# Optimization experiments

Measured on AMD Instinct MI355X. Metric: run time of the kernel, lower is better.

The kernel has to match this reference:

```python
import jax, jax.numpy as jnp
import numpy as np

B, N, D = 256, 256, 256
DELTA_BEARING = 5.0
DELTA_HEADING = 5.0
N_HEAD = int(360 / DELTA_HEADING)   # 72
N_BEAR = int(360 / DELTA_BEARING)   # 72
DOMAIN_PARAM = 2.0
EPS = 1e-14


def setup_inputs() -> dict:
    key = jax.random.key(0)
    ks = jax.random.split(key, 8)
    hidden_state = jax.random.normal(ks[0], (B, N, D), dtype=jnp.float32)
    distance_matrix = jax.random.uniform(ks[1], (B, N, N), dtype=jnp.float32) * 10.0
    bearing_matrix = jax.random.uniform(ks[2], (B, N, N), dtype=jnp.float32) * 360.0
    heading_matrix = jax.random.uniform(ks[3], (B, N, N), dtype=jnp.float32) * 360.0
    sequence_mask = (jax.random.uniform(ks[4], (B, N)) > 0.1).astype(jnp.float32)
    domain = jnp.full((N_HEAD, N_BEAR), DOMAIN_PARAM, dtype=jnp.float32)
    lim = 1.0 / np.sqrt(2 * D)
    W = jax.random.uniform(ks[5], (D, 2 * D), minval=-lim, maxval=lim, dtype=jnp.float32)
    b = jax.random.uniform(ks[6], (D,), minval=-lim, maxval=lim, dtype=jnp.float32)
    return {"hidden_state": hidden_state, "distance_matrix": distance_matrix,
            "bearing_matrix": bearing_matrix, "heading_matrix": heading_matrix,
            "sequence_mask": sequence_mask, "domain": domain, "W": W, "b": b}


def _compute_weights(domain, distance_matrix, bearing_matrix, heading_matrix, sequence_mask):
    # domain lookup indices from heading/bearing bins
    idx1 = jnp.clip(jnp.floor((heading_matrix + DELTA_HEADING / 2) / DELTA_HEADING), 0, N_HEAD - 1).astype(jnp.int32)
    idx2 = jnp.clip(jnp.floor((bearing_matrix + DELTA_BEARING / 2) / DELTA_BEARING), 0, N_BEAR - 1).astype(jnp.int32)
    w = jax.nn.relu(domain[idx1, idx2] - distance_matrix)  # (B,N,N)
    # pairwise sequence mask and no-self-attention mask
    wm = sequence_mask[:, :, None] * sequence_mask[:, None, :]  # (B,N,N)
    ped = 1.0 - jnp.eye(w.shape[1], dtype=w.dtype)               # (N,N)
    valid = (ped[None, :, :] * wm) > 0
    w = jnp.where(valid, w, 0.0)
    # masked softmax over dim=2: zeros are treated as masked, epsilon-stabilized
    mask = (w != 0).astype(w.dtype)
    masked_exps = jnp.exp(w) * mask + EPS
    w = masked_exps / (masked_exps.sum(axis=2, keepdims=True) + EPS)
    return jnp.where(valid, w, 0.0)


def reference(hidden_state, distance_matrix, bearing_matrix, heading_matrix, sequence_mask, domain, W, b):
    weights = _compute_weights(domain, distance_matrix, bearing_matrix, heading_matrix, sequence_mask)
    weighted_hidden = jnp.einsum('bij,bjd->bid', weights, hidden_state)  # (B,N,D)
    cat = jnp.concatenate([weighted_hidden, hidden_state], axis=-1)       # (B,N,2D)
    return jnp.einsum('bnk,dk->bnd', cat, W) + b
```

## Files before the change

### kernel.cpp

```cpp
#include <hip/hip_runtime.h>
#include <hip/hip_bf16.h>


typedef __attribute__((ext_vector_type(4))) float  f32x4;
typedef __attribute__((ext_vector_type(8))) short  bf16x8;
typedef __attribute__((ext_vector_type(4))) short  bf16x4;

#define EPSC 1e-14f

__device__ __forceinline__ short f2bf(float v) {
  __hip_bfloat16 h = __float2bfloat16(v);
  return *reinterpret_cast<short*>(&h);
}

__global__ void k0_pack(const float* __restrict__ W, short* __restrict__ Wbf) {
  int idx = blockIdx.x * 256 + threadIdx.x;
  f32x4 v = *(const f32x4*)(W + (size_t)idx * 4);
  bf16x4 pk;
  pk[0] = f2bf(v[0]); pk[1] = f2bf(v[1]); pk[2] = f2bf(v[2]); pk[3] = f2bf(v[3]);
  *(bf16x4*)(Wbf + (size_t)idx * 4) = pk;
}

__global__ __launch_bounds__(512) void k1_proj(
    const float* __restrict__ H, const short* __restrict__ Wbf,
    short* __restrict__ P1T) {
  extern __shared__ char sm[];
  char* sA = sm;
  char* sB = sm + 9216;
  const int t  = threadIdx.x;
  const int n0 = blockIdx.x * 64;
  const int b  = n0 >> 8;
  const int jb = n0 & 255;

  const int wid = t >> 6, l = t & 63;
  const int wn = wid >> 2, wc = wid & 3;
  const int lr = l & 15, lg = l >> 4;
  f32x4 acc[2][4] = {};

  for (int kk = 0; kk < 256; kk += 64) {
    __syncthreads();
    #pragma unroll
    for (int p = 0; p < 2; ++p) {
      int q = t + 512 * p;
      int j = q >> 4, seg = q & 15;
      f32x4 hv = *(const f32x4*)(H + ((size_t)(n0 + j)) * 256 + kk + seg * 4);
      bf16x4 pk;
      pk[0] = f2bf(hv[0]); pk[1] = f2bf(hv[1]); pk[2] = f2bf(hv[2]); pk[3] = f2bf(hv[3]);
      *(bf16x4*)(sA + j * 144 + seg * 8) = pk;
    }
    #pragma unroll
    for (int p = 0; p < 4; ++p) {
      int z = t + 512 * p;
      int d = z >> 3, s = z & 7;
      bf16x8 v = *(const bf16x8*)(Wbf + (size_t)d * 512 + kk + s * 8);
      *(bf16x8*)(sB + d * 144 + s * 16) = v;
    }
    __syncthreads();
    #pragma unroll
    for (int sub = 0; sub < 2; ++sub) {
      bf16x8 a[2], bb[4];
      #pragma unroll
      for (int m = 0; m < 2; ++m) {
        int row = wn * 32 + m * 16 + lr;
        a[m] = *(const bf16x8*)(sA + row * 144 + sub * 64 + lg * 16);
      }
      #pragma unroll
      for (int f = 0; f < 4; ++f) {
        int d = wc * 64 + f * 16 + lr;
        bb[f] = *(const bf16x8*)(sB + d * 144 + sub * 64 + lg * 16);
      }
      #pragma unroll
      for (int m = 0; m < 2; ++m) {
        #pragma unroll
        for (int f = 0; f < 4; ++f)
          acc[m][f] = __builtin_amdgcn_mfma_f32_16x16x32_bf16(a[m], bb[f], acc[m][f], 0, 0, 0);
      }
    }
  }

  #pragma unroll
  for (int m = 0; m < 2; ++m) {
    int jl = wn * 32 + m * 16 + lg * 4;
    #pragma unroll
    for (int f = 0; f < 4; ++f) {
      int d = wc * 64 + f * 16 + lr;
      f32x4 v = acc[m][f];
      bf16x4 pk;
      pk[0] = f2bf(v[0]); pk[1] = f2bf(v[1]); pk[2] = f2bf(v[2]); pk[3] = f2bf(v[3]);
      *(bf16x4*)(P1T + (size_t)b * 65536 + (size_t)d * 256 + jb + jl) = pk;
    }
  }
}

__global__ __launch_bounds__(512, 4) void k2_fused(
    const float* __restrict__ dist, const float* __restrict__ bear,
    const float* __restrict__ head, const float* __restrict__ seqmask,
    const float* __restrict__ domain, const short* __restrict__ P1T,
    const short* __restrict__ Wbf, const float* __restrict__ H,
    const float* __restrict__ bias, float* __restrict__ out) {
  extern __shared__ char sm[];
  char*  sB    = sm;
  char*  sA    = sm + 36864;
  float* sDom  = (float*)(sm + 55296);
  float* sMask = (float*)(sm + 76032);
  float* sBias = (float*)(sm + 77056);
  const int t  = threadIdx.x;
  const int b  = blockIdx.x >> 1;
  const int i0 = (blockIdx.x & 1) * 128;

  for (int x = t; x < 72 * 72; x += 512) sDom[x] = domain[x];
  if (t < 256) { sMask[t] = seqmask[b * 256 + t]; sBias[t] = bias[t]; }
  __syncthreads();

  const int wid = t >> 6, l = t & 63;
  const int lr = l & 15, lg = l >> 4;
  const int i  = i0 + wid * 16 + lr;
  const float mI = sMask[i];
  const size_t base = ((size_t)b * 256 + i) * 256;

  f32x4 acc[16] = {};
  float rs = 0.f;

  for (int c = 0; c < 4; ++c) {
    const int kk = c * 64;
    bf16x8 st[4];
    #pragma unroll
    for (int p = 0; p < 4; ++p) {
      int z = t + 512 * p;
      st[p] = *(const bf16x8*)(P1T + (size_t)b * 65536 + (size_t)(z >> 3) * 256 + kk + (z & 7) * 8);
    }
    bf16x8 afrag[2];
    #pragma unroll
    for (int sub = 0; sub < 2; ++sub) {
      const int k0 = kk + sub * 32 + lg * 8;
      f32x4 d0 = *(const f32x4*)(dist + base + k0);
      f32x4 d1 = *(const f32x4*)(dist + base + k0 + 4);
      f32x4 b0 = *(const f32x4*)(bear + base + k0);
      f32x4 b1 = *(const f32x4*)(bear + base + k0 + 4);
      f32x4 h0 = *(const f32x4*)(head + base + k0);
      f32x4 h1 = *(const f32x4*)(head + base + k0 + 4);
      f32x4 m0 = *(const f32x4*)(sMask + k0);
      f32x4 m1 = *(const f32x4*)(sMask + k0 + 4);
      bf16x8 pk;
      #pragma unroll
      for (int e = 0; e < 4; ++e) {
        float f1 = fminf(fmaxf(floorf((h0[e] + 2.5f) * 0.2f), 0.f), 71.f);
        float f2 = fminf(fmaxf(floorf((b0[e] + 2.5f) * 0.2f), 0.f), 71.f);
        float wv = fmaxf(sDom[(int)(f1 * 72.f + f2)] - d0[e], 0.f);
        bool valid = (i != k0 + e) && (mI != 0.f) && (m0[e] != 0.f);
        float ex = (wv > 0.f) ? __expf(wv) : 0.f;
        ex = valid ? ex : 0.f;
        rs += ex;
        pk[e] = f2bf(valid ? (ex + EPSC) : 0.f);
      }
      #pragma unroll
      for (int e = 0; e < 4; ++e) {
        float f1 = fminf(fmaxf(floorf((h1[e] + 2.5f) * 0.2f), 0.f), 71.f);
        float f2 = fminf(fmaxf(floorf((b1[e] + 2.5f) * 0.2f), 0.f), 71.f);
        float wv = fmaxf(sDom[(int)(f1 * 72.f + f2)] - d1[e], 0.f);
        bool valid = (i != k0 + 4 + e) && (mI != 0.f) && (m1[e] != 0.f);
        float ex = (wv > 0.f) ? __expf(wv) : 0.f;
        ex = valid ? ex : 0.f;
        rs += ex;
        pk[4 + e] = f2bf(valid ? (ex + EPSC) : 0.f);
      }
      afrag[sub] = pk;
    }
    #pragma unroll
    for (int p = 0; p < 4; ++p) {
      int z = t + 512 * p;
      *(bf16x8*)(sB + (z >> 3) * 144 + (z & 7) * 16) = st[p];
    }
    __syncthreads();
    #pragma unroll
    for (int sub = 0; sub < 2; ++sub) {
      #pragma unroll
      for (int n = 0; n < 16; ++n) {
        bf16x8 bb = *(const bf16x8*)(sB + (n * 16 + lr) * 144 + sub * 64 + lg * 16);
        acc[n] = __builtin_amdgcn_mfma_f32_16x16x32_bf16(afrag[sub], bb, acc[n], 0, 0, 0);
      }
    }
    __syncthreads();
  }

  rs += __shfl_xor(rs, 16, 64);
  rs += __shfl_xor(rs, 32, 64);
  const float scale = 1.0f / (rs + 257.0f * EPSC);
  float srow[4];
  #pragma unroll
  for (int r = 0; r < 4; ++r) srow[r] = __shfl(scale, lg * 4 + r, 64);
  #pragma unroll
  for (int n = 0; n < 16; ++n) {
    acc[n][0] *= srow[0]; acc[n][1] *= srow[1];
    acc[n][2] *= srow[2]; acc[n][3] *= srow[3];
  }

  for (int c = 0; c < 4; ++c) {
    const int kk = c * 64;
    #pragma unroll
    for (int p = 0; p < 2; ++p) {
      int z = t + 512 * p;
      int row = z >> 3, s = z & 7;
      const float* src = H + ((size_t)b * 256 + i0 + row) * 256 + kk + s * 8;
      f32x4 x0 = *(const f32x4*)src;
      f32x4 x1 = *(const f32x4*)(src + 4);
      bf16x8 pk;
      pk[0] = f2bf(x0[0]); pk[1] = f2bf(x0[1]); pk[2] = f2bf(x0[2]); pk[3] = f2bf(x0[3]);
      pk[4] = f2bf(x1[0]); pk[5] = f2bf(x1[1]); pk[6] = f2bf(x1[2]); pk[7] = f2bf(x1[3]);
      *(bf16x8*)(sA + row * 144 + s * 16) = pk;
    }
    #pragma unroll
    for (int p = 0; p < 4; ++p) {
      int z = t + 512 * p;
      bf16x8 v = *(const bf16x8*)(Wbf + (size_t)(z >> 3) * 512 + 256 + kk + (z & 7) * 8);
      *(bf16x8*)(sB + (z >> 3) * 144 + (z & 7) * 16) = v;
    }
    __syncthreads();
    #pragma unroll
    for (int sub = 0; sub < 2; ++sub) {
      bf16x8 av = *(const bf16x8*)(sA + (wid * 16 + lr) * 144 + sub * 64 + lg * 16);
      #pragma unroll
      for (int n = 0; n < 16; ++n) {
        bf16x8 bb = *(const bf16x8*)(sB + (n * 16 + lr) * 144 + sub * 64 + lg * 16);
        acc[n] = __builtin_amdgcn_mfma_f32_16x16x32_bf16(av, bb, acc[n], 0, 0, 0);
      }
    }
    __syncthreads();
  }

  #pragma unroll
  for (int n = 0; n < 16; ++n) {
    int d = n * 16 + lr;
    float bs = sBias[d];
    #pragma unroll
    for (int r = 0; r < 4; ++r) {
      int row = wid * 16 + lg * 4 + r;
      out[((size_t)b * 256 + i0 + row) * 256 + d] = acc[n][r] + bs;
    }
  }
}

extern "C" void kernel_launch(void* const* d_in, const int* in_sizes, int n_in,
                              void* d_out, int out_size, void* d_ws, size_t ws_size,
                              hipStream_t stream) {
  const float* hidden  = (const float*)d_in[0];
  const float* dist    = (const float*)d_in[1];
  const float* bear    = (const float*)d_in[2];
  const float* head    = (const float*)d_in[3];
  const float* seqmask = (const float*)d_in[4];
  const float* domain  = (const float*)d_in[5];
  const float* W       = (const float*)d_in[6];
  const float* bias    = (const float*)d_in[7];
  float* out = (float*)d_out;

  char* ws = (char*)d_ws;
  short* Wbf = (short*)ws;
  short* P1T = (short*)(ws + (1u << 20));

  k0_pack<<<128, 256, 0, stream>>>(W, Wbf);
  k1_proj<<<1024, 512, 46080, stream>>>(hidden, Wbf, P1T);
  k2_fused<<<512, 512, 78080, stream>>>(dist, bear, head, seqmask, domain,
                                        P1T, Wbf, hidden, bias, out);
}
```

Measured before the change: 122.5 us.

## Drop LDS staging in fused kernel, load MFMA B operands directly from global

The fused weights-and-projection kernel no longer stages P1T, W and H tiles through shared memory with barriers. Each wave now reads its MFMA B fragments straight from global memory (relying on L2/L1 caching) and converts H rows to bf16 in registers. Blocks shrink from 512 to 256 threads over 64 rows, with much smaller LDS use, so more blocks can be resident. The cost is redundant, less coalesced global and L2 traffic for the B operands across waves and blocks.

```diff
diff --git a/kernel.cpp b/kernel.cpp
--- a/kernel.cpp
+++ b/kernel.cpp
@@ -92,24 +92,23 @@
   }
 }
 
-__global__ __launch_bounds__(512, 4) void k2_fused(
+__global__ __launch_bounds__(256) void k2_fused(
     const float* __restrict__ dist, const float* __restrict__ bear,
     const float* __restrict__ head, const float* __restrict__ seqmask,
     const float* __restrict__ domain, const short* __restrict__ P1T,
     const short* __restrict__ Wbf, const float* __restrict__ H,
     const float* __restrict__ bias, float* __restrict__ out) {
   extern __shared__ char sm[];
-  char*  sB    = sm;
-  char*  sA    = sm + 36864;
-  float* sDom  = (float*)(sm + 55296);
-  float* sMask = (float*)(sm + 76032);
-  float* sBias = (float*)(sm + 77056);
+  float* sDom  = (float*)sm;
+  float* sMask = (float*)(sm + 20736);
+  float* sBias = (float*)(sm + 21760);
   const int t  = threadIdx.x;
-  const int b  = blockIdx.x >> 1;
-  const int i0 = (blockIdx.x & 1) * 128;
-
-  for (int x = t; x < 72 * 72; x += 512) sDom[x] = domain[x];
-  if (t < 256) { sMask[t] = seqmask[b * 256 + t]; sBias[t] = bias[t]; }
+  const int b  = blockIdx.x >> 2;
+  const int i0 = (blockIdx.x & 3) * 64;
+
+  for (int x = t; x < 72 * 72; x += 256) sDom[x] = domain[x];
+  sMask[t] = seqmask[b * 256 + t];
+  sBias[t] = bias[t];
   __syncthreads();
 
   const int wid = t >> 6, l = t & 63;
@@ -117,19 +116,13 @@
   const int i  = i0 + wid * 16 + lr;
   const float mI = sMask[i];
   const size_t base = ((size_t)b * 256 + i) * 256;
+  const short* __restrict__ P1b = P1T + (size_t)b * 65536;
 
   f32x4 acc[16] = {};
   float rs = 0.f;
 
   for (int c = 0; c < 4; ++c) {
     const int kk = c * 64;
-    bf16x8 st[4];
-    #pragma unroll
-    for (int p = 0; p < 4; ++p) {
-      int z = t + 512 * p;
-      st[p] = *(const bf16x8*)(P1T + (size_t)b * 65536 + (size_t)(z >> 3) * 256 + kk + (z & 7) * 8);
-    }
-    bf16x8 afrag[2];
     #pragma unroll
     for (int sub = 0; sub < 2; ++sub) {
       const int k0 = kk + sub * 32 + lg * 8;
@@ -164,23 +157,13 @@
         rs += ex;
         pk[4 + e] = f2bf(valid ? (ex + EPSC) : 0.f);
       }
-      afrag[sub] = pk;
-    }
-    #pragma unroll
-    for (int p = 0; p < 4; ++p) {
-      int z = t + 512 * p;
-      *(bf16x8*)(sB + (z >> 3) * 144 + (z & 7) * 16) = st[p];
-    }
-    __syncthreads();
-    #pragma unroll
-    for (int sub = 0; sub < 2; ++sub) {
+      const short* bp = P1b + kk + sub * 32 + lg * 8;
       #pragma unroll
       for (int n = 0; n < 16; ++n) {
-        bf16x8 bb = *(const bf16x8*)(sB + (n * 16 + lr) * 144 + sub * 64 + lg * 16);
-        acc[n] = __builtin_amdgcn_mfma_f32_16x16x32_bf16(afrag[sub], bb, acc[n], 0, 0, 0);
-      }
-    }
-    __syncthreads();
+        bf16x8 bb = *(const bf16x8*)(bp + (size_t)(n * 16 + lr) * 256);
+        acc[n] = __builtin_amdgcn_mfma_f32_16x16x32_bf16(pk, bb, acc[n], 0, 0, 0);
+      }
+    }
   }
 
   rs += __shfl_xor(rs, 16, 64);
@@ -198,34 +181,20 @@
   for (int c = 0; c < 4; ++c) {
     const int kk = c * 64;
     #pragma unroll
-    for (int p = 0; p < 2; ++p) {
-      int z = t + 512 * p;
-      int row = z >> 3, s = z & 7;
-      const float* src = H + ((size_t)b * 256 + i0 + row) * 256 + kk + s * 8;
-      f32x4 x0 = *(const f32x4*)src;
-      f32x4 x1 = *(const f32x4*)(src + 4);
-      bf16x8 pk;
-      pk[0] = f2bf(x0[0]); pk[1] = f2bf(x0[1]); pk[2] = f2bf(x0[2]); pk[3] = f2bf(x0[3]);
-      pk[4] = f2bf(x1[0]); pk[5] = f2bf(x1[1]); pk[6] = f2bf(x1[2]); pk[7] = f2bf(x1[3]);
-      *(bf16x8*)(sA + row * 144 + s * 16) = pk;
-    }
-    #pragma unroll
-    for (int p = 0; p < 4; ++p) {
-      int z = t + 512 * p;
-      bf16x8 v = *(const bf16x8*)(Wbf + (size_t)(z >> 3) * 512 + 256 + kk + (z & 7) * 8);
-      *(bf16x8*)(sB + (z >> 3) * 144 + (z & 7) * 16) = v;
-    }
-    __syncthreads();
-    #pragma unroll
     for (int sub = 0; sub < 2; ++sub) {
-      bf16x8 av = *(const bf16x8*)(sA + (wid * 16 + lr) * 144 + sub * 64 + lg * 16);
+      const int k0 = kk + sub * 32 + lg * 8;
+      f32x4 x0 = *(const f32x4*)(H + base + k0);
+      f32x4 x1 = *(const f32x4*)(H + base + k0 + 4);
+      bf16x8 av;
+      av[0] = f2bf(x0[0]); av[1] = f2bf(x0[1]); av[2] = f2bf(x0[2]); av[3] = f2bf(x0[3]);
+      av[4] = f2bf(x1[0]); av[5] = f2bf(x1[1]); av[6] = f2bf(x1[2]); av[7] = f2bf(x1[3]);
+      const short* bp = Wbf + 256 + kk + sub * 32 + lg * 8;
       #pragma unroll
       for (int n = 0; n < 16; ++n) {
-        bf16x8 bb = *(const bf16x8*)(sB + (n * 16 + lr) * 144 + sub * 64 + lg * 16);
+        bf16x8 bb = *(const bf16x8*)(bp + (size_t)(n * 16 + lr) * 512);
         acc[n] = __builtin_amdgcn_mfma_f32_16x16x32_bf16(av, bb, acc[n], 0, 0, 0);
       }
     }
-    __syncthreads();
   }
 
   #pragma unroll
@@ -234,8 +203,8 @@
     float bs = sBias[d];
     #pragma unroll
     for (int r = 0; r < 4; ++r) {
-      int row = wid * 16 + lg * 4 + r;
-      out[((size_t)b * 256 + i0 + row) * 256 + d] = acc[n][r] + bs;
+      int row = i0 + wid * 16 + lg * 4 + r;
+      out[((size_t)b * 256 + row) * 256 + d] = acc[n][r] + bs;
     }
   }
 }
@@ -259,6 +228,6 @@
 
   k0_pack<<<128, 256, 0, stream>>>(W, Wbf);
   k1_proj<<<1024, 512, 46080, stream>>>(hidden, Wbf, P1T);
-  k2_fused<<<512, 512, 78080, stream>>>(dist, bear, head, seqmask, domain,
-                                        P1T, Wbf, hidden, bias, out);
-}
+  k2_fused<<<1024, 256, 22784, stream>>>(dist, bear, head, seqmask, domain,
+                                         P1T, Wbf, hidden, bias, out);
+}
```

New measurement: 226.3 us. 84.7% more time.
